# Kernel optimization log

Measured on AMD Instinct MI355X. Metric: run time of the kernel, lower is better.

## Reference

```python
import jax, jax.numpy as jnp
import numpy as np

N_NODES = 50000
N_EDGES = 800000
N_GRAPHS = 64
IN_DIM, HID_DIM, OUT_DIM = 64, 128, 3


def setup_inputs() -> dict:
    key = jax.random.key(0)
    ks = jax.random.split(key, 8)
    x = jax.random.normal(ks[0], (N_NODES, IN_DIM), dtype=jnp.float32)
    edge_index = jax.random.randint(ks[1], (2, N_EDGES), 0, N_NODES, dtype=jnp.int64)
    batch = jnp.sort(jax.random.randint(ks[2], (N_NODES,), 0, N_GRAPHS, dtype=jnp.int64))
    # Glorot-ish init for weights, zero biases (matches GCNConv/Linear defaults in spirit)
    W1 = jax.random.normal(ks[3], (IN_DIM, HID_DIM), dtype=jnp.float32) / np.sqrt(IN_DIM)
    b1 = jnp.zeros((HID_DIM,), dtype=jnp.float32)
    W2 = jax.random.normal(ks[4], (HID_DIM, HID_DIM), dtype=jnp.float32) / np.sqrt(HID_DIM)
    b2 = jnp.zeros((HID_DIM,), dtype=jnp.float32)
    Wf = jax.random.normal(ks[5], (HID_DIM, OUT_DIM), dtype=jnp.float32) / np.sqrt(HID_DIM)
    bf = jnp.zeros((OUT_DIM,), dtype=jnp.float32)
    return {"x": x, "edge_index": edge_index, "batch": batch,
            "W1": W1, "b1": b1, "W2": W2, "b2": b2, "Wf": Wf, "bf": bf}


def _gcn_conv(x, src, dst, norm, W, b, n_nodes):
    # PyG GCNConv: h = X W; out_i = sum_{j->i} norm_ij * h_j + b
    h = x @ W                                  # [N, D_out]
    msg = h[src] * norm[:, None]               # gather + scale  [E+N, D_out]
    out = jax.ops.segment_sum(msg, dst, num_segments=n_nodes)  # scatter-add
    return out + b


def reference(x, edge_index, batch, W1, b1, W2, b2, Wf, bf):
    n_nodes = x.shape[0]
    loops = jnp.arange(n_nodes, dtype=edge_index.dtype)
    src = jnp.concatenate([edge_index[0], loops])  # add self-loops
    dst = jnp.concatenate([edge_index[1], loops])
    # Symmetric normalization: deg over destinations (incl. self-loops)
    deg = jax.ops.segment_sum(jnp.ones_like(dst, dtype=x.dtype), dst, num_segments=n_nodes)
    dinv = jax.lax.rsqrt(jnp.maximum(deg, 1.0))
    norm = dinv[src] * dinv[dst]               # [E+N]

    h = jax.nn.relu(_gcn_conv(x, src, dst, norm, W1, b1, n_nodes))
    h = jax.nn.relu(_gcn_conv(h, src, dst, norm, W2, b2, n_nodes))

    # global_mean_pool over batch ids
    sums = jax.ops.segment_sum(h, batch, num_segments=N_GRAPHS)        # [G, H]
    counts = jax.ops.segment_sum(jnp.ones((n_nodes,), h.dtype), batch, num_segments=N_GRAPHS)
    pooled = sums / jnp.maximum(counts, 1.0)[:, None]

    return pooled @ Wf + bf                    # [G, OUT_DIM]
```

## Files before the change

### kernel.cpp

```cpp
#include <hip/hip_runtime.h>

constexpr int NN = 50000;
constexpr int NE = 800000;
constexpr int NG = 64;
constexpr int DI = 64;
constexpr int DH = 128;
constexpr int DO = 3;

constexpr int SCAN_B = 256;
constexpr int NBK = 196;
constexpr int CHUNK = 4096;
constexpr int NCH = (NE + CHUNK - 1) / CHUNK;
constexpr int BBTOT = NBK * NCH;
constexpr int NBB = (BBTOT + 255) / 256;

typedef unsigned int u32;

__device__ inline float blo(u32 u) { return __uint_as_float(u << 16); }
__device__ inline float bhi(u32 u) { return __uint_as_float(u & 0xffff0000u); }
__device__ inline u32 f2b(float f) {
    u32 u = __float_as_uint(f);
    return (u + 0x7fffu + ((u >> 16) & 1u)) >> 16;
}
__device__ inline void fma8(float w, uint4 v, float acc[8]) {
    acc[0] = fmaf(w, blo(v.x), acc[0]); acc[1] = fmaf(w, bhi(v.x), acc[1]);
    acc[2] = fmaf(w, blo(v.y), acc[2]); acc[3] = fmaf(w, bhi(v.y), acc[3]);
    acc[4] = fmaf(w, blo(v.z), acc[4]); acc[5] = fmaf(w, bhi(v.z), acc[5]);
    acc[6] = fmaf(w, blo(v.w), acc[6]); acc[7] = fmaf(w, bhi(v.w), acc[7]);
}

__global__ void k_init(const float* __restrict__ x, uint4* __restrict__ xb,
                       float* __restrict__ pooled, const int* __restrict__ batch,
                       int* __restrict__ gstart) {
    int i = blockIdx.x * blockDim.x + threadIdx.x;
    if (i < NN * DI / 8) {
        float4 a = reinterpret_cast<const float4*>(x)[i * 2];
        float4 b = reinterpret_cast<const float4*>(x)[i * 2 + 1];
        uint4 o;
        o.x = f2b(a.x) | (f2b(a.y) << 16);
        o.y = f2b(a.z) | (f2b(a.w) << 16);
        o.z = f2b(b.x) | (f2b(b.y) << 16);
        o.w = f2b(b.z) | (f2b(b.w) << 16);
        xb[i] = o;
    }
    if (i < NG * DH) pooled[i] = 0.0f;
    if (blockIdx.x == 0 && threadIdx.x <= NG) {
        int g = threadIdx.x;
        int lo = 0, hi = NN;
        while (lo < hi) {
            int mid = (lo + hi) >> 1;
            if (batch[mid] < g) lo = mid + 1; else hi = mid;
        }
        gstart[g] = lo;
    }
}

__global__ __launch_bounds__(256) void k_histc(const int* __restrict__ dst,
                                               int* __restrict__ cntBB) {
    __shared__ int lcnt[NBK];
    const int t = threadIdx.x, c = blockIdx.x;
    for (int b = t; b < NBK; b += 256) lcnt[b] = 0;
    __syncthreads();
    const int base = c * CHUNK;
    const int endE = min(base + CHUNK, NE);
    for (int e = base + t; e < endE; e += 256) atomicAdd(&lcnt[dst[e] >> 8], 1);
    __syncthreads();
    for (int b = t; b < NBK; b += 256) cntBB[b * NCH + c] = lcnt[b];
}

__device__ inline void blockScan(int* sm) {
    for (int off = 1; off < SCAN_B; off <<= 1) {
        int add = (threadIdx.x >= off) ? sm[threadIdx.x - off] : 0;
        __syncthreads();
        sm[threadIdx.x] += add;
        __syncthreads();
    }
}

__global__ void k_scanBB1(int* __restrict__ cntBB, int* __restrict__ bbpartial) {
    __shared__ int sm[SCAN_B];
    int i = blockIdx.x * SCAN_B + threadIdx.x;
    int v = (i < BBTOT) ? cntBB[i] : 0;
    sm[threadIdx.x] = v;
    __syncthreads();
    blockScan(sm);
    if (i < BBTOT) cntBB[i] = sm[threadIdx.x] - v;
    if (threadIdx.x == SCAN_B - 1) bbpartial[blockIdx.x] = sm[SCAN_B - 1];
}

__global__ void k_scanB(int* __restrict__ bbpartial) {
    __shared__ int sm[SCAN_B];
    int v = (threadIdx.x < NBB) ? bbpartial[threadIdx.x] : 0;
    sm[threadIdx.x] = v;
    __syncthreads();
    blockScan(sm);
    if (threadIdx.x < NBB) bbpartial[threadIdx.x] = sm[threadIdx.x] - v;
}

__global__ __launch_bounds__(256) void k_fillP2(const int* __restrict__ src,
                                                const int* __restrict__ dst,
                                                const int* __restrict__ cntBB,
                                                const int* __restrict__ bbpartial,
                                                u32* __restrict__ stage) {
    __shared__ int lcur[NBK];
    const int t = threadIdx.x, c = blockIdx.x;
    for (int b = t; b < NBK; b += 256) {
        int i = b * NCH + c;
        lcur[b] = cntBB[i] + bbpartial[i >> 8];
    }
    __syncthreads();
    const int base = c * CHUNK;
    const int endE = min(base + CHUNK, NE);
    for (int e = base + t; e < endE; e += 256) {
        int s = src[e], d = dst[e];
        int slot = atomicAdd(&lcur[d >> 8], 1);
        stage[slot] = ((u32)(d & 255) << 16) | (u32)s;
    }
}

__global__ __launch_bounds__(256) void k_fillB(const u32* __restrict__ stage,
                                               const int* __restrict__ cntBB,
                                               const int* __restrict__ bbpartial,
                                               int* __restrict__ rowptr,
                                               float* __restrict__ dinv,
                                               ushort* __restrict__ csr16) {
    __shared__ int cnt[256];
    __shared__ int sm[256];
    __shared__ int cur[256];
    const int b = blockIdx.x, t = threadIdx.x;
    cnt[t] = 0;
    const int i0 = b * NCH;
    const int beg = cntBB[i0] + bbpartial[i0 >> 8];
    const int end = (b + 1 < NBK) ? cntBB[i0 + NCH] + bbpartial[(i0 + NCH) >> 8] : NE;
    __syncthreads();
    for (int i = beg + t; i < end; i += 256) atomicAdd(&cnt[(stage[i] >> 16) & 255u], 1);
    __syncthreads();
    const int v = cnt[t];
    sm[t] = v;
    __syncthreads();
    blockScan(sm);
    const int excl = sm[t] - v;
    const int n = b * 256 + t;
    if (n < NN) {
        rowptr[n] = beg + excl;
        dinv[n] = rsqrtf((float)(v + 1));
    }
    if (b == NBK - 1 && t == 0) rowptr[NN] = NE;
    cur[t] = beg + excl;
    __syncthreads();
    for (int i = beg + t; i < end; i += 256) {
        u32 e = stage[i];
        int slot = atomicAdd(&cur[(e >> 16) & 255u], 1);
        csr16[slot] = (ushort)(e & 0xffffu);
    }
}

__device__ inline float4 fmaf4(float s, float4 w, float4 a) {
    a.x = fmaf(s, w.x, a.x); a.y = fmaf(s, w.y, a.y);
    a.z = fmaf(s, w.z, a.z); a.w = fmaf(s, w.w, a.w);
    return a;
}

__global__ __launch_bounds__(256) void k_aggemm12(const ushort* __restrict__ xb,
                                                  const ushort* __restrict__ csr16,
                                                  const int* __restrict__ rowptr,
                                                  const float* __restrict__ dinv,
                                                  const float* __restrict__ W1,
                                                  const float* __restrict__ b1,
                                                  const float* __restrict__ W2,
                                                  u32* __restrict__ T) {
    constexpr int AP = DI + 4;
    constexpr int HP = DH + 4;
    constexpr int KT = 32;
    __shared__ float sAH[64 * HP];
    __shared__ float sW[KT * DH];
    const int t = threadIdx.x;
    const int row0 = blockIdx.x * 64;

    {
        const int sub = t >> 3;
        const int sl = t & 7;
#pragma unroll
        for (int rep = 0; rep < 2; ++rep) {
            const int lr = sub + rep * 32;
            const int node = row0 + lr;
            float acc[8] = {0.f, 0.f, 0.f, 0.f, 0.f, 0.f, 0.f, 0.f};
            if (node < NN) {
                const float dn = dinv[node];
                uint4 v = *reinterpret_cast<const uint4*>(xb + (size_t)node * DI + sl * 8);
                float ws = dn * dn;
                acc[0] = ws * blo(v.x); acc[1] = ws * bhi(v.x);
                acc[2] = ws * blo(v.y); acc[3] = ws * bhi(v.y);
                acc[4] = ws * blo(v.z); acc[5] = ws * bhi(v.z);
                acc[6] = ws * blo(v.w); acc[7] = ws * bhi(v.w);
                int j = rowptr[node];
                const int end = rowptr[node + 1];
                while ((j & 3) && j < end) {
                    int s = csr16[j];
                    uint4 g = *reinterpret_cast<const uint4*>(xb + (size_t)s * DI + sl * 8);
                    fma8(dn * dinv[s], g, acc);
                    ++j;
                }
                for (; j + 4 <= end; j += 4) {
                    ushort4 q = *reinterpret_cast<const ushort4*>(csr16 + j);
                    uint4 g0 = *reinterpret_cast<const uint4*>(xb + (size_t)q.x * DI + sl * 8);
                    uint4 g1 = *reinterpret_cast<const uint4*>(xb + (size_t)q.y * DI + sl * 8);
                    uint4 g2 = *reinterpret_cast<const uint4*>(xb + (size_t)q.z * DI + sl * 8);
                    uint4 g3 = *reinterpret_cast<const uint4*>(xb + (size_t)q.w * DI + sl * 8);
                    float w0 = dn * dinv[q.x], w1 = dn * dinv[q.y];
                    float w2 = dn * dinv[q.z], w3 = dn * dinv[q.w];
                    fma8(w0, g0, acc);
                    fma8(w1, g1, acc);
                    fma8(w2, g2, acc);
                    fma8(w3, g3, acc);
                }
                while (j < end) {
                    int s = csr16[j];
                    uint4 g = *reinterpret_cast<const uint4*>(xb + (size_t)s * DI + sl * 8);
                    fma8(dn * dinv[s], g, acc);
                    ++j;
                }
            }
            *reinterpret_cast<float4*>(&sAH[lr * AP + sl * 8]) =
                make_float4(acc[0], acc[1], acc[2], acc[3]);
            *reinterpret_cast<float4*>(&sAH[lr * AP + sl * 8 + 4]) =
                make_float4(acc[4], acc[5], acc[6], acc[7]);
        }
    }

    const int cg = t & 31;
    const int rg = t >> 5;
    float4 acc[8];
#pragma unroll
    for (int j = 0; j < 8; ++j) acc[j] = make_float4(0.f, 0.f, 0.f, 0.f);

#pragma unroll
    for (int tile = 0; tile < 2; ++tile) {
        __syncthreads();
        {
            const float4* Wg = reinterpret_cast<const float4*>(W1 + tile * KT * DH);
            float4* sW4 = reinterpret_cast<float4*>(sW);
#pragma unroll
            for (int i = 0; i < 4; ++i) sW4[t + 256 * i] = Wg[t + 256 * i];
        }
        __syncthreads();
#pragma unroll 2
        for (int kk = 0; kk < KT; kk += 4) {
            float4 w0 = *reinterpret_cast<const float4*>(&sW[(kk + 0) * DH + cg * 4]);
            float4 w1 = *reinterpret_cast<const float4*>(&sW[(kk + 1) * DH + cg * 4]);
            float4 w2 = *reinterpret_cast<const float4*>(&sW[(kk + 2) * DH + cg * 4]);
            float4 w3 = *reinterpret_cast<const float4*>(&sW[(kk + 3) * DH + cg * 4]);
#pragma unroll
            for (int j = 0; j < 8; ++j) {
                float4 a = *reinterpret_cast<const float4*>(&sAH[(rg * 8 + j) * AP + tile * KT + kk]);
                acc[j] = fmaf4(a.x, w0, acc[j]);
                acc[j] = fmaf4(a.y, w1, acc[j]);
                acc[j] = fmaf4(a.z, w2, acc[j]);
                acc[j] = fmaf4(a.w, w3, acc[j]);
            }
        }
    }
    {
        float4 bb = *reinterpret_cast<const float4*>(b1 + cg * 4);
#pragma unroll
        for (int j = 0; j < 8; ++j) {
            acc[j].x = fmaxf(acc[j].x + bb.x, 0.f);
            acc[j].y = fmaxf(acc[j].y + bb.y, 0.f);
            acc[j].z = fmaxf(acc[j].z + bb.z, 0.f);
            acc[j].w = fmaxf(acc[j].w + bb.w, 0.f);
        }
    }

    __syncthreads();
#pragma unroll
    for (int j = 0; j < 8; ++j)
        *reinterpret_cast<float4*>(&sAH[(rg * 8 + j) * HP + cg * 4]) = acc[j];

    float4 acc2[8];
#pragma unroll
    for (int j = 0; j < 8; ++j) acc2[j] = make_float4(0.f, 0.f, 0.f, 0.f);

#pragma unroll
    for (int tile = 0; tile < 4; ++tile) {
        __syncthreads();
        {
            const float4* Wg = reinterpret_cast<const float4*>(W2 + tile * KT * DH);
            float4* sW4 = reinterpret_cast<float4*>(sW);
#pragma unroll
            for (int i = 0; i < 4; ++i) sW4[t + 256 * i] = Wg[t + 256 * i];
        }
        __syncthreads();
#pragma unroll 2
        for (int kk = 0; kk < KT; kk += 4) {
            float4 w0 = *reinterpret_cast<const float4*>(&sW[(kk + 0) * DH + cg * 4]);
            float4 w1 = *reinterpret_cast<const float4*>(&sW[(kk + 1) * DH + cg * 4]);
            float4 w2 = *reinterpret_cast<const float4*>(&sW[(kk + 2) * DH + cg * 4]);
            float4 w3 = *reinterpret_cast<const float4*>(&sW[(kk + 3) * DH + cg * 4]);
#pragma unroll
            for (int j = 0; j < 8; ++j) {
                float4 a = *reinterpret_cast<const float4*>(&sAH[(rg * 8 + j) * HP + tile * KT + kk]);
                acc2[j] = fmaf4(a.x, w0, acc2[j]);
                acc2[j] = fmaf4(a.y, w1, acc2[j]);
                acc2[j] = fmaf4(a.z, w2, acc2[j]);
                acc2[j] = fmaf4(a.w, w3, acc2[j]);
            }
        }
    }
#pragma unroll
    for (int j = 0; j < 8; ++j) {
        int gr = row0 + rg * 8 + j;
        if (gr < NN) {
            uint2 o = make_uint2(f2b(acc2[j].x) | (f2b(acc2[j].y) << 16),
                                 f2b(acc2[j].z) | (f2b(acc2[j].w) << 16));
            *reinterpret_cast<uint2*>(&T[(size_t)gr * (DH / 2) + cg * 2]) = o;
        }
    }
}

__global__ __launch_bounds__(256) void k_aggd(const ushort* __restrict__ hb,
                                              const ushort* __restrict__ csr16,
                                              const int* __restrict__ rowptr,
                                              const float* __restrict__ dinv,
                                              const float* __restrict__ bias,
                                              u32* __restrict__ out) {
    constexpr int SUB = DH / 8;
    constexpr int NPB = 256 / SUB;
    const int sub = threadIdx.x / SUB;
    const int sl = threadIdx.x % SUB;
    const int node = blockIdx.x * NPB + sub;
    if (node >= NN) return;

    const float dn = dinv[node];
    float acc[8];
    {
        uint4 v = *reinterpret_cast<const uint4*>(hb + (size_t)node * DH + sl * 8);
        float w = dn * dn;
        acc[0] = w * blo(v.x); acc[1] = w * bhi(v.x);
        acc[2] = w * blo(v.y); acc[3] = w * bhi(v.y);
        acc[4] = w * blo(v.z); acc[5] = w * bhi(v.z);
        acc[6] = w * blo(v.w); acc[7] = w * bhi(v.w);
    }
    int j = rowptr[node];
    const int end = rowptr[node + 1];
    while ((j & 3) && j < end) {
        int s = csr16[j];
        uint4 g = *reinterpret_cast<const uint4*>(hb + (size_t)s * DH + sl * 8);
        fma8(dn * dinv[s], g, acc);
        ++j;
    }
    for (; j + 4 <= end; j += 4) {
        ushort4 q = *reinterpret_cast<const ushort4*>(csr16 + j);
        uint4 g0 = *reinterpret_cast<const uint4*>(hb + (size_t)q.x * DH + sl * 8);
        uint4 g1 = *reinterpret_cast<const uint4*>(hb + (size_t)q.y * DH + sl * 8);
        uint4 g2 = *reinterpret_cast<const uint4*>(hb + (size_t)q.z * DH + sl * 8);
        uint4 g3 = *reinterpret_cast<const uint4*>(hb + (size_t)q.w * DH + sl * 8);
        float w0 = dn * dinv[q.x], w1 = dn * dinv[q.y];
        float w2 = dn * dinv[q.z], w3 = dn * dinv[q.w];
        fma8(w0, g0, acc);
        fma8(w1, g1, acc);
        fma8(w2, g2, acc);
        fma8(w3, g3, acc);
    }
    while (j < end) {
        int s = csr16[j];
        uint4 g = *reinterpret_cast<const uint4*>(hb + (size_t)s * DH + sl * 8);
        fma8(dn * dinv[s], g, acc);
        ++j;
    }
    {
        float4 b0 = *reinterpret_cast<const float4*>(bias + sl * 8);
        float4 b1v = *reinterpret_cast<const float4*>(bias + sl * 8 + 4);
        acc[0] = fmaxf(acc[0] + b0.x, 0.f); acc[1] = fmaxf(acc[1] + b0.y, 0.f);
        acc[2] = fmaxf(acc[2] + b0.z, 0.f); acc[3] = fmaxf(acc[3] + b0.w, 0.f);
        acc[4] = fmaxf(acc[4] + b1v.x, 0.f); acc[5] = fmaxf(acc[5] + b1v.y, 0.f);
        acc[6] = fmaxf(acc[6] + b1v.z, 0.f); acc[7] = fmaxf(acc[7] + b1v.w, 0.f);
    }
    uint4 o;
    o.x = f2b(acc[0]) | (f2b(acc[1]) << 16);
    o.y = f2b(acc[2]) | (f2b(acc[3]) << 16);
    o.z = f2b(acc[4]) | (f2b(acc[5]) << 16);
    o.w = f2b(acc[6]) | (f2b(acc[7]) << 16);
    *reinterpret_cast<uint4*>(reinterpret_cast<ushort*>(out) + (size_t)node * DH + sl * 8) = o;
}

constexpr int POOL_CHUNK = 64;
__global__ __launch_bounds__(256) void k_pool3(const u32* __restrict__ h2b,
                                               const int* __restrict__ batch,
                                               float* __restrict__ pooled) {
    const int c2 = threadIdx.x & 63;
    const int q = threadIdx.x >> 6;
    const int n0 = blockIdx.x * POOL_CHUNK;
    const int nEnd = min(n0 + POOL_CHUNK, NN);
    float a0 = 0.f, a1 = 0.f;
    int gcur = -1;
    for (int n = n0 + q; n < nEnd; n += 4) {
        int g = batch[n];
        if (g != gcur) {
            if (gcur >= 0) {
                atomicAdd(&pooled[gcur * DH + c2 * 2], a0);
                atomicAdd(&pooled[gcur * DH + c2 * 2 + 1], a1);
            }
            a0 = a1 = 0.f;
            gcur = g;
        }
        u32 v = h2b[(size_t)n * (DH / 2) + c2];
        a0 += blo(v);
        a1 += bhi(v);
    }
    if (gcur >= 0) {
        atomicAdd(&pooled[gcur * DH + c2 * 2], a0);
        atomicAdd(&pooled[gcur * DH + c2 * 2 + 1], a1);
    }
}

__global__ void k_head(const float* __restrict__ pooled, const int* __restrict__ gstart,
                       const float* __restrict__ Wf, const float* __restrict__ bf,
                       float* __restrict__ out) {
    int t = threadIdx.x;
    if (t >= NG * DO) return;
    int g = t / DO, o = t - g * DO;
    float acc = 0.0f;
    for (int k = 0; k < DH; ++k) acc += pooled[g * DH + k] * Wf[k * DO + o];
    float cnt = fmaxf((float)(gstart[g + 1] - gstart[g]), 1.0f);
    out[t] = acc / cnt + bf[o];
}

extern "C" void kernel_launch(void* const* d_in, const int* in_sizes, int n_in,
                              void* d_out, int out_size, void* d_ws, size_t ws_size,
                              hipStream_t stream) {
    const float* x   = (const float*)d_in[0];
    const int* ei    = (const int*)d_in[1];
    const int* batch = (const int*)d_in[2];
    const float* W1  = (const float*)d_in[3];
    const float* b1  = (const float*)d_in[4];
    const float* W2  = (const float*)d_in[5];
    const float* b2  = (const float*)d_in[6];
    const float* Wf  = (const float*)d_in[7];
    const float* bf  = (const float*)d_in[8];
    float* out = (float*)d_out;

    const int* src = ei;
    const int* dst = ei + NE;

    int* rowptr    = (int*)d_ws;
    int* bbpartial = rowptr + 50056;
    int* gstart    = bbpartial + 256;
    int* cntBB     = gstart + 80;
    ushort* csr16  = (ushort*)(cntBB + 38416);
    float* dinv    = (float*)((u32*)(cntBB + 38416) + 400000);
    u32* xbu       = (u32*)(dinv + 50048);
    u32* stage     = xbu + 1600000;
    u32* tbu       = stage + 800000;
    u32* h2b       = tbu + 3200000;
    float* pooled  = (float*)(h2b + 3200000);

    ushort* xb = (ushort*)xbu;
    ushort* tb = (ushort*)tbu;

    const int B = 256;
    k_init<<<(NN * DI / 8 + B - 1) / B, B, 0, stream>>>(x, (uint4*)xb, pooled, batch, gstart);
    k_histc<<<NCH, 256, 0, stream>>>(dst, cntBB);
    k_scanBB1<<<NBB, SCAN_B, 0, stream>>>(cntBB, bbpartial);
    k_scanB<<<1, SCAN_B, 0, stream>>>(bbpartial);
    k_fillP2<<<NCH, 256, 0, stream>>>(src, dst, cntBB, bbpartial, stage);
    k_fillB<<<NBK, 256, 0, stream>>>(stage, cntBB, bbpartial, rowptr, dinv, csr16);

    const int gemmGrid = (NN + 63) / 64;

    k_aggemm12<<<gemmGrid, 256, 0, stream>>>(xb, csr16, rowptr, dinv, W1, b1, W2, tbu);

    k_aggd<<<(NN + 15) / 16, 256, 0, stream>>>(tb, csr16, rowptr, dinv, b2, h2b);

    k_pool3<<<(NN + POOL_CHUNK - 1) / POOL_CHUNK, 256, 0, stream>>>(h2b, batch, pooled);
    k_head<<<1, 256, 0, stream>>>(pooled, gstart, Wf, bf, out);
}
```

Baseline: 174.3 us.

## Split layer-1 aggregation out of fused GEMM kernel; store hidden in bf16 LDS

```diff
diff --git a/kernel.cpp b/kernel.cpp
--- a/kernel.cpp
+++ b/kernel.cpp
@@ -155,81 +155,110 @@
     }
 }
 
+template <int D, bool BIAS_RELU>
+__global__ __launch_bounds__(256) void k_agge(const ushort* __restrict__ hb,
+                                              const ushort* __restrict__ csr16,
+                                              const int* __restrict__ rowptr,
+                                              const float* __restrict__ dinv,
+                                              const float* __restrict__ bias,
+                                              u32* __restrict__ out) {
+    constexpr int SUB = D / 8;
+    constexpr int NPB = 256 / SUB;
+    const int sub = threadIdx.x / SUB;
+    const int sl = threadIdx.x % SUB;
+    const int node = blockIdx.x * NPB + sub;
+    if (node >= NN) return;
+
+    const float dn = dinv[node];
+    float acc[8];
+    {
+        uint4 v = *reinterpret_cast<const uint4*>(hb + (size_t)node * D + sl * 8);
+        float w = dn * dn;
+        acc[0] = w * blo(v.x); acc[1] = w * bhi(v.x);
+        acc[2] = w * blo(v.y); acc[3] = w * bhi(v.y);
+        acc[4] = w * blo(v.z); acc[5] = w * bhi(v.z);
+        acc[6] = w * blo(v.w); acc[7] = w * bhi(v.w);
+    }
+    int j = rowptr[node];
+    const int end = rowptr[node + 1];
+    while ((j & 3) && j < end) {
+        int s = csr16[j];
+        uint4 g = *reinterpret_cast<const uint4*>(hb + (size_t)s * D + sl * 8);
+        fma8(dn * dinv[s], g, acc);
+        ++j;
+    }
+    for (; j + 4 <= end; j += 4) {
+        ushort4 q = *reinterpret_cast<const ushort4*>(csr16 + j);
+        uint4 g0 = *reinterpret_cast<const uint4*>(hb + (size_t)q.x * D + sl * 8);
+        uint4 g1 = *reinterpret_cast<const uint4*>(hb + (size_t)q.y * D + sl * 8);
+        uint4 g2 = *reinterpret_cast<const uint4*>(hb + (size_t)q.z * D + sl * 8);
+        uint4 g3 = *reinterpret_cast<const uint4*>(hb + (size_t)q.w * D + sl * 8);
+        float w0 = dn * dinv[q.x], w1 = dn * dinv[q.y];
+        float w2 = dn * dinv[q.z], w3 = dn * dinv[q.w];
+        fma8(w0, g0, acc);
+        fma8(w1, g1, acc);
+        fma8(w2, g2, acc);
+        fma8(w3, g3, acc);
+    }
+    while (j < end) {
+        int s = csr16[j];
+        uint4 g = *reinterpret_cast<const uint4*>(hb + (size_t)s * D + sl * 8);
+        fma8(dn * dinv[s], g, acc);
+        ++j;
+    }
+    if (BIAS_RELU) {
+        float4 b0 = *reinterpret_cast<const float4*>(bias + sl * 8);
+        float4 b1v = *reinterpret_cast<const float4*>(bias + sl * 8 + 4);
+        acc[0] = fmaxf(acc[0] + b0.x, 0.f); acc[1] = fmaxf(acc[1] + b0.y, 0.f);
+        acc[2] = fmaxf(acc[2] + b0.z, 0.f); acc[3] = fmaxf(acc[3] + b0.w, 0.f);
+        acc[4] = fmaxf(acc[4] + b1v.x, 0.f); acc[5] = fmaxf(acc[5] + b1v.y, 0.f);
+        acc[6] = fmaxf(acc[6] + b1v.z, 0.f); acc[7] = fmaxf(acc[7] + b1v.w, 0.f);
+    }
+    uint4 o;
+    o.x = f2b(acc[0]) | (f2b(acc[1]) << 16);
+    o.y = f2b(acc[2]) | (f2b(acc[3]) << 16);
+    o.z = f2b(acc[4]) | (f2b(acc[5]) << 16);
+    o.w = f2b(acc[6]) | (f2b(acc[7]) << 16);
+    *reinterpret_cast<uint4*>(reinterpret_cast<ushort*>(out) + (size_t)node * D + sl * 8) = o;
+}
+
 __device__ inline float4 fmaf4(float s, float4 w, float4 a) {
     a.x = fmaf(s, w.x, a.x); a.y = fmaf(s, w.y, a.y);
     a.z = fmaf(s, w.z, a.z); a.w = fmaf(s, w.w, a.w);
     return a;
 }
 
-__global__ __launch_bounds__(256) void k_aggemm12(const ushort* __restrict__ xb,
-                                                  const ushort* __restrict__ csr16,
-                                                  const int* __restrict__ rowptr,
-                                                  const float* __restrict__ dinv,
-                                                  const float* __restrict__ W1,
-                                                  const float* __restrict__ b1,
-                                                  const float* __restrict__ W2,
-                                                  u32* __restrict__ T) {
+__global__ __launch_bounds__(256) void k_gemm12(const ushort* __restrict__ A,
+                                                const float* __restrict__ W1,
+                                                const float* __restrict__ b1,
+                                                const float* __restrict__ W2,
+                                                u32* __restrict__ T) {
     constexpr int AP = DI + 4;
-    constexpr int HP = DH + 4;
     constexpr int KT = 32;
-    __shared__ float sAH[64 * HP];
+    __shared__ float sA[64 * AP];
     __shared__ float sW[KT * DH];
+    ushort* sH = reinterpret_cast<ushort*>(sA);
     const int t = threadIdx.x;
     const int row0 = blockIdx.x * 64;
-
-    {
-        const int sub = t >> 3;
-        const int sl = t & 7;
-#pragma unroll
-        for (int rep = 0; rep < 2; ++rep) {
-            const int lr = sub + rep * 32;
-            const int node = row0 + lr;
-            float acc[8] = {0.f, 0.f, 0.f, 0.f, 0.f, 0.f, 0.f, 0.f};
-            if (node < NN) {
-                const float dn = dinv[node];
-                uint4 v = *reinterpret_cast<const uint4*>(xb + (size_t)node * DI + sl * 8);
-                float ws = dn * dn;
-                acc[0] = ws * blo(v.x); acc[1] = ws * bhi(v.x);
-                acc[2] = ws * blo(v.y); acc[3] = ws * bhi(v.y);
-                acc[4] = ws * blo(v.z); acc[5] = ws * bhi(v.z);
-                acc[6] = ws * blo(v.w); acc[7] = ws * bhi(v.w);
-                int j = rowptr[node];
-                const int end = rowptr[node + 1];
-                while ((j & 3) && j < end) {
-                    int s = csr16[j];
-                    uint4 g = *reinterpret_cast<const uint4*>(xb + (size_t)s * DI + sl * 8);
-                    fma8(dn * dinv[s], g, acc);
-                    ++j;
-                }
-                for (; j + 4 <= end; j += 4) {
-                    ushort4 q = *reinterpret_cast<const ushort4*>(csr16 + j);
-                    uint4 g0 = *reinterpret_cast<const uint4*>(xb + (size_t)q.x * DI + sl * 8);
-                    uint4 g1 = *reinterpret_cast<const uint4*>(xb + (size_t)q.y * DI + sl * 8);
-                    uint4 g2 = *reinterpret_cast<const uint4*>(xb + (size_t)q.z * DI + sl * 8);
-                    uint4 g3 = *reinterpret_cast<const uint4*>(xb + (size_t)q.w * DI + sl * 8);
-                    float w0 = dn * dinv[q.x], w1 = dn * dinv[q.y];
-                    float w2 = dn * dinv[q.z], w3 = dn * dinv[q.w];
-                    fma8(w0, g0, acc);
-                    fma8(w1, g1, acc);
-                    fma8(w2, g2, acc);
-                    fma8(w3, g3, acc);
-                }
-                while (j < end) {
-                    int s = csr16[j];
-                    uint4 g = *reinterpret_cast<const uint4*>(xb + (size_t)s * DI + sl * 8);
-                    fma8(dn * dinv[s], g, acc);
-                    ++j;
-                }
-            }
-            *reinterpret_cast<float4*>(&sAH[lr * AP + sl * 8]) =
-                make_float4(acc[0], acc[1], acc[2], acc[3]);
-            *reinterpret_cast<float4*>(&sAH[lr * AP + sl * 8 + 4]) =
-                make_float4(acc[4], acc[5], acc[6], acc[7]);
-        }
-    }
-
     const int cg = t & 31;
     const int rg = t >> 5;
+
+    {
+        const int row = t >> 2;
+        const int q2 = (t & 3) * 2;
+        int gr = row0 + row;
+#pragma unroll
+        for (int u = 0; u < 2; ++u) {
+            uint4 v = make_uint4(0u, 0u, 0u, 0u);
+            if (gr < NN)
+                v = *reinterpret_cast<const uint4*>(A + (size_t)gr * DI + (q2 + u) * 8);
+            *reinterpret_cast<float4*>(&sA[row * AP + (q2 + u) * 8]) =
+                make_float4(blo(v.x), bhi(v.x), blo(v.y), bhi(v.y));
+            *reinterpret_cast<float4*>(&sA[row * AP + (q2 + u) * 8 + 4]) =
+                make_float4(blo(v.z), bhi(v.z), blo(v.w), bhi(v.w));
+        }
+    }
+
     float4 acc[8];
 #pragma unroll
     for (int j = 0; j < 8; ++j) acc[j] = make_float4(0.f, 0.f, 0.f, 0.f);
@@ -252,7 +281,7 @@
             float4 w3 = *reinterpret_cast<const float4*>(&sW[(kk + 3) * DH + cg * 4]);
 #pragma unroll
             for (int j = 0; j < 8; ++j) {
-                float4 a = *reinterpret_cast<const float4*>(&sAH[(rg * 8 + j) * AP + tile * KT + kk]);
+                float4 a = *reinterpret_cast<const float4*>(&sA[(rg * 8 + j) * AP + tile * KT + kk]);
                 acc[j] = fmaf4(a.x, w0, acc[j]);
                 acc[j] = fmaf4(a.y, w1, acc[j]);
                 acc[j] = fmaf4(a.z, w2, acc[j]);
@@ -273,8 +302,11 @@
 
     __syncthreads();
 #pragma unroll
-    for (int j = 0; j < 8; ++j)
-        *reinterpret_cast<float4*>(&sAH[(rg * 8 + j) * HP + cg * 4]) = acc[j];
+    for (int j = 0; j < 8; ++j) {
+        uint2 o = make_uint2(f2b(acc[j].x) | (f2b(acc[j].y) << 16),
+                             f2b(acc[j].z) | (f2b(acc[j].w) << 16));
+        *reinterpret_cast<uint2*>(&sH[(rg * 8 + j) * DH + cg * 4]) = o;
+    }
 
     float4 acc2[8];
 #pragma unroll
@@ -298,11 +330,11 @@
             float4 w3 = *reinterpret_cast<const float4*>(&sW[(kk + 3) * DH + cg * 4]);
 #pragma unroll
             for (int j = 0; j < 8; ++j) {
-                float4 a = *reinterpret_cast<const float4*>(&sAH[(rg * 8 + j) * HP + tile * KT + kk]);
-                acc2[j] = fmaf4(a.x, w0, acc2[j]);
-                acc2[j] = fmaf4(a.y, w1, acc2[j]);
-                acc2[j] = fmaf4(a.z, w2, acc2[j]);
-                acc2[j] = fmaf4(a.w, w3, acc2[j]);
+                uint2 av = *reinterpret_cast<const uint2*>(&sH[(rg * 8 + j) * DH + tile * KT + kk]);
+                acc2[j] = fmaf4(blo(av.x), w0, acc2[j]);
+                acc2[j] = fmaf4(bhi(av.x), w1, acc2[j]);
+                acc2[j] = fmaf4(blo(av.y), w2, acc2[j]);
+                acc2[j] = fmaf4(bhi(av.y), w3, acc2[j]);
             }
         }
     }
@@ -315,72 +347,6 @@
             *reinterpret_cast<uint2*>(&T[(size_t)gr * (DH / 2) + cg * 2]) = o;
         }
     }
-}
-
-__global__ __launch_bounds__(256) void k_aggd(const ushort* __restrict__ hb,
-                                              const ushort* __restrict__ csr16,
-                                              const int* __restrict__ rowptr,
-                                              const float* __restrict__ dinv,
-                                              const float* __restrict__ bias,
-                                              u32* __restrict__ out) {
-    constexpr int SUB = DH / 8;
-    constexpr int NPB = 256 / SUB;
-    const int sub = threadIdx.x / SUB;
-    const int sl = threadIdx.x % SUB;
-    const int node = blockIdx.x * NPB + sub;
-    if (node >= NN) return;
-
-    const float dn = dinv[node];
-    float acc[8];
-    {
-        uint4 v = *reinterpret_cast<const uint4*>(hb + (size_t)node * DH + sl * 8);
-        float w = dn * dn;
-        acc[0] = w * blo(v.x); acc[1] = w * bhi(v.x);
-        acc[2] = w * blo(v.y); acc[3] = w * bhi(v.y);
-        acc[4] = w * blo(v.z); acc[5] = w * bhi(v.z);
-        acc[6] = w * blo(v.w); acc[7] = w * bhi(v.w);
-    }
-    int j = rowptr[node];
-    const int end = rowptr[node + 1];
-    while ((j & 3) && j < end) {
-        int s = csr16[j];
-        uint4 g = *reinterpret_cast<const uint4*>(hb + (size_t)s * DH + sl * 8);
-        fma8(dn * dinv[s], g, acc);
-        ++j;
-    }
-    for (; j + 4 <= end; j += 4) {
-        ushort4 q = *reinterpret_cast<const ushort4*>(csr16 + j);
-        uint4 g0 = *reinterpret_cast<const uint4*>(hb + (size_t)q.x * DH + sl * 8);
-        uint4 g1 = *reinterpret_cast<const uint4*>(hb + (size_t)q.y * DH + sl * 8);
-        uint4 g2 = *reinterpret_cast<const uint4*>(hb + (size_t)q.z * DH + sl * 8);
-        uint4 g3 = *reinterpret_cast<const uint4*>(hb + (size_t)q.w * DH + sl * 8);
-        float w0 = dn * dinv[q.x], w1 = dn * dinv[q.y];
-        float w2 = dn * dinv[q.z], w3 = dn * dinv[q.w];
-        fma8(w0, g0, acc);
-        fma8(w1, g1, acc);
-        fma8(w2, g2, acc);
-        fma8(w3, g3, acc);
-    }
-    while (j < end) {
-        int s = csr16[j];
-        uint4 g = *reinterpret_cast<const uint4*>(hb + (size_t)s * DH + sl * 8);
-        fma8(dn * dinv[s], g, acc);
-        ++j;
-    }
-    {
-        float4 b0 = *reinterpret_cast<const float4*>(bias + sl * 8);
-        float4 b1v = *reinterpret_cast<const float4*>(bias + sl * 8 + 4);
-        acc[0] = fmaxf(acc[0] + b0.x, 0.f); acc[1] = fmaxf(acc[1] + b0.y, 0.f);
-        acc[2] = fmaxf(acc[2] + b0.z, 0.f); acc[3] = fmaxf(acc[3] + b0.w, 0.f);
-        acc[4] = fmaxf(acc[4] + b1v.x, 0.f); acc[5] = fmaxf(acc[5] + b1v.y, 0.f);
-        acc[6] = fmaxf(acc[6] + b1v.z, 0.f); acc[7] = fmaxf(acc[7] + b1v.w, 0.f);
-    }
-    uint4 o;
-    o.x = f2b(acc[0]) | (f2b(acc[1]) << 16);
-    o.y = f2b(acc[2]) | (f2b(acc[3]) << 16);
-    o.z = f2b(acc[4]) | (f2b(acc[5]) << 16);
-    o.w = f2b(acc[6]) | (f2b(acc[7]) << 16);
-    *reinterpret_cast<uint4*>(reinterpret_cast<ushort*>(out) + (size_t)node * DH + sl * 8) = o;
 }
 
 constexpr int POOL_CHUNK = 64;
@@ -450,12 +416,14 @@
     float* dinv    = (float*)((u32*)(cntBB + 38416) + 400000);
     u32* xbu       = (u32*)(dinv + 50048);
     u32* stage     = xbu + 1600000;
-    u32* tbu       = stage + 800000;
+    u32* agg1bu    = stage + 800000;
+    u32* tbu       = agg1bu + 1600000;
     u32* h2b       = tbu + 3200000;
     float* pooled  = (float*)(h2b + 3200000);
 
-    ushort* xb = (ushort*)xbu;
-    ushort* tb = (ushort*)tbu;
+    ushort* xb    = (ushort*)xbu;
+    ushort* agg1b = (ushort*)agg1bu;
+    ushort* tb    = (ushort*)tbu;
 
     const int B = 256;
     k_init<<<(NN * DI / 8 + B - 1) / B, B, 0, stream>>>(x, (uint4*)xb, pooled, batch, gstart);
@@ -467,9 +435,11 @@
 
     const int gemmGrid = (NN + 63) / 64;
 
-    k_aggemm12<<<gemmGrid, 256, 0, stream>>>(xb, csr16, rowptr, dinv, W1, b1, W2, tbu);
-
-    k_aggd<<<(NN + 15) / 16, 256, 0, stream>>>(tb, csr16, rowptr, dinv, b2, h2b);
+    k_agge<DI, false><<<(NN + 31) / 32, 256, 0, stream>>>(xb, csr16, rowptr, dinv,
+                                                          nullptr, agg1bu);
+    k_gemm12<<<gemmGrid, 256, 0, stream>>>(agg1b, W1, b1, W2, tbu);
+
+    k_agge<DH, true><<<(NN + 15) / 16, 256, 0, stream>>>(tb, csr16, rowptr, dinv, b2, h2b);
 
     k_pool3<<<(NN + POOL_CHUNK - 1) / POOL_CHUNK, 256, 0, stream>>>(h2b, batch, pooled);
     k_head<<<1, 256, 0, stream>>>(pooled, gstart, Wf, bf, out);
```

Result: faster. 168.1 us (-3.6%).
